# Optimization experiments

Hardware: AMD Instinct MI355X
Metric: run time of the kernel (lower is better)

## Reference

```python
import jax, jax.numpy as jnp
import numpy as np


def _morpho(x, weight, bias, sign, padding, stride):
    # x: [B,C,H,W], weight: [B,C,kh,kw], bias: [B,C], sign: [B]
    B, C, H, W = x.shape
    kh, kw = weight.shape[-2:]
    # sign handling: if |sign| >= 1e-7 multiply by sign, else leave unchanged
    m = (jnp.abs(sign) >= 1e-7).astype(x.dtype)          # [B], constant (detached in torch)
    s = m * sign + (1.0 - m)                              # effective multiplier per sample
    xs = x * s[:, None, None, None]
    # unfold zero-pads, and sign*0 == 0, so padding signed x with zeros is equivalent
    xp = jnp.pad(xs, ((0, 0), (0, 0), (padding, padding), (padding, padding)))
    H2 = (H + 2 * padding - kh) // stride + 1
    W2 = (W + 2 * padding - kw) // stride + 1
    # direct windowed max-plus: y[b,c,i,j] = max_{p,q} xs_pad[b,c,i*s+p,j*s+q] + w[b,c,p,q]
    # small fixed kh*kw loop avoids materializing the B*C*kh*kw*L unfold tensor
    y = jnp.full((B, C, H2, W2), -jnp.inf, dtype=x.dtype)
    for p in range(kh):
        for q in range(kw):
            patch = jax.lax.slice(
                xp,
                (0, 0, p, q),
                (B, C, p + (H2 - 1) * stride + 1, q + (W2 - 1) * stride + 1),
                (1, 1, stride, stride),
            )  # [B,C,H2,W2]
            y = jnp.maximum(y, patch + weight[:, :, p, q][:, :, None, None])
    y = y + bias[:, :, None, None]
    return y * s[:, None, None, None]


def setup_inputs() -> dict:
    key = jax.random.key(0)
    k1, k2, k3, k4 = jax.random.split(key, 4)
    B, C, H, W, kh, kw = 16, 64, 128, 128, 5, 5
    return {
        "x": jax.random.normal(k1, (B, C, H, W), dtype=jnp.float32),
        "weight": jax.random.normal(k2, (B, C, kh, kw), dtype=jnp.float32) * 0.1,
        "bias": jax.random.normal(k3, (B, C), dtype=jnp.float32) * 0.1,
        "sign": jax.random.normal(k4, (B,), dtype=jnp.float32),
        "padding": 2,
        "stride": 1,
    }


def reference(x, weight, bias, sign, padding, stride):
    return _morpho(x, weight, bias, sign, padding, stride)
```

## Files before the change

### kernel.cpp

```cpp
#include <hip/hip_runtime.h>
#include <math.h>
#include <stdint.h>

#define HH 128
#define WW 128
#define NFLOATS (16 * 64 * HH * WW)

typedef __fp16 h2 __attribute__((ext_vector_type(2)));

__device__ __forceinline__ h2 h2max(h2 a, h2 b) { return __builtin_elementwise_max(a, b); }
__device__ __forceinline__ uint32_t h2u(h2 v) { return __builtin_bit_cast(uint32_t, v); }
__device__ __forceinline__ h2 uh2(uint32_t v) { return __builtin_bit_cast(h2, v); }

#if __has_builtin(__builtin_elementwise_fma)
#define H2FMA(a, b, c) __builtin_elementwise_fma((a), (b), (c))
#else
#define H2FMA(a, b, c) ((a) * (b) + (c))
#endif

#define WAITV(n) do { asm volatile("s_waitcnt vmcnt(" #n ")" ::: "memory"); \
                      __builtin_amdgcn_sched_barrier(0); } while (0)

__global__ __launch_bounds__(256) void morpho_kernel(
    const float* __restrict__ x,
    const float* __restrict__ wgt,
    const float* __restrict__ bias,
    const float* __restrict__ sign,
    float* __restrict__ out)
{
    const int bid  = blockIdx.x;
    const int blk  = (bid & 7) * 512 + (bid >> 3);
    const int quad = blk & 3;
    const int bc   = blk >> 2;
    const int b    = bc >> 6;

    float*       __restrict__ yp = out + (size_t)bc * (HH * WW);
    const float* __restrict__ wp = wgt + bc * 25;

    const float sgn = sign[b];
    const float s   = (fabsf(sgn) >= 1e-7f) ? sgn : 1.0f;
    const float bvs = bias[bc] * s;
    const __fp16 sh = (__fp16)s;
    const h2 s2 = { sh, sh };

    uint32_t wsu[25];
#pragma unroll
    for (int k = 0; k < 25; ++k) {
        const __fp16 wh = (__fp16)wp[k];
        h2 w2 = { wh, wh };
        wsu[k] = (uint32_t)__builtin_amdgcn_readfirstlane((int)h2u(w2));
    }

    const int t  = threadIdx.x;
    const int tx = t & 31;
    const int ty = t >> 5;
    const int j0 = tx * 4;
    const int i0 = quad * 32 + ty * 4;
    const int planeOff = bc * (HH * WW);
    const bool mL = (tx > 0);
    const bool mR = (tx < 31);

    float2 vl[8]; float4 vm[8]; float2 vr[8];
    h2 acc0[4], acc1[4];

    auto ISSUE = [&](int r8) {
        const int rrow = i0 - 2 + r8;
        const int rc = min(max(rrow, 0), HH - 1);
        const int oM = planeOff + rc * WW + j0;
        const int oL = max(oM - 2, 0);
        const int oR = min(oM + 4, NFLOATS - 2);
        asm volatile("global_load_dwordx2 %0, %1, off" : "=v"(vl[r8]) : "v"(x + oL));
        asm volatile("global_load_dwordx4 %0, %1, off" : "=v"(vm[r8]) : "v"(x + oM));
        asm volatile("global_load_dwordx2 %0, %1, off" : "=v"(vr[r8]) : "v"(x + oR));
    };

    auto CONSUME = [&](int r8) {
        const int  rrow = i0 - 2 + r8;
        const bool rv = ((unsigned)rrow < (unsigned)HH);
        uint32_t e0 = h2u(__builtin_amdgcn_cvt_pkrtz(vl[r8].x, vl[r8].y));
        uint32_t e1 = h2u(__builtin_amdgcn_cvt_pkrtz(vm[r8].x, vm[r8].y));
        uint32_t e2 = h2u(__builtin_amdgcn_cvt_pkrtz(vm[r8].z, vm[r8].w));
        uint32_t e3 = h2u(__builtin_amdgcn_cvt_pkrtz(vr[r8].x, vr[r8].y));
        e0 = (rv && mL) ? e0 : 0u;
        e1 = rv ? e1 : 0u;
        e2 = rv ? e2 : 0u;
        e3 = (rv && mR) ? e3 : 0u;
        const uint32_t o0 = __builtin_amdgcn_alignbit(e1, e0, 16);
        const uint32_t o1 = __builtin_amdgcn_alignbit(e2, e1, 16);
        const uint32_t o2 = __builtin_amdgcn_alignbit(e3, e2, 16);
        const uint32_t P0[5] = { e0, o0, e1, o1, e2 };
        const uint32_t P1[5] = { e1, o1, e2, o2, e3 };
#pragma unroll
        for (int p = 0; p < 5; ++p) {
            const int oi = r8 - p;
            if (oi >= 0 && oi < 4) {
                const h2 w0 = uh2(wsu[p * 5 + 0]);
                const h2 w1 = uh2(wsu[p * 5 + 1]);
                const h2 w2 = uh2(wsu[p * 5 + 2]);
                const h2 w3 = uh2(wsu[p * 5 + 3]);
                const h2 w4 = uh2(wsu[p * 5 + 4]);
                {
                    const h2 t0 = H2FMA(uh2(P0[0]), s2, w0);
                    const h2 t1 = H2FMA(uh2(P0[1]), s2, w1);
                    const h2 t2 = H2FMA(uh2(P0[2]), s2, w2);
                    const h2 t3 = H2FMA(uh2(P0[3]), s2, w3);
                    const h2 t4 = H2FMA(uh2(P0[4]), s2, w4);
                    h2 mm = h2max(h2max(h2max(t0, t1), h2max(t2, t3)), t4);
                    acc0[oi] = (p == 0) ? mm : h2max(acc0[oi], mm);
                }
                {
                    const h2 t0 = H2FMA(uh2(P1[0]), s2, w0);
                    const h2 t1 = H2FMA(uh2(P1[1]), s2, w1);
                    const h2 t2 = H2FMA(uh2(P1[2]), s2, w2);
                    const h2 t3 = H2FMA(uh2(P1[3]), s2, w3);
                    const h2 t4 = H2FMA(uh2(P1[4]), s2, w4);
                    h2 mm = h2max(h2max(h2max(t0, t1), h2max(t2, t3)), t4);
                    acc1[oi] = (p == 0) ? mm : h2max(acc1[oi], mm);
                }
            }
        }
    };

    ISSUE(0); ISSUE(1); ISSUE(2); ISSUE(3);
    WAITV(9); CONSUME(0); ISSUE(4);
    WAITV(9); CONSUME(1); ISSUE(5);
    WAITV(9); CONSUME(2); ISSUE(6);
    WAITV(9); CONSUME(3); ISSUE(7);
    WAITV(9); CONSUME(4);
    WAITV(6); CONSUME(5);
    WAITV(3); CONSUME(6);
    WAITV(0); CONSUME(7);

#pragma unroll
    for (int a = 0; a < 4; ++a) {
        float4 o;
        o.x = fmaf((float)acc0[a][0], s, bvs);
        o.y = fmaf((float)acc0[a][1], s, bvs);
        o.z = fmaf((float)acc1[a][0], s, bvs);
        o.w = fmaf((float)acc1[a][1], s, bvs);
        *reinterpret_cast<float4*>(yp + (size_t)(i0 + a) * WW + j0) = o;
    }
}

extern "C" void kernel_launch(void* const* d_in, const int* in_sizes, int n_in,
                              void* d_out, int out_size, void* d_ws, size_t ws_size,
                              hipStream_t stream) {
    (void)d_ws; (void)ws_size; (void)in_sizes; (void)n_in; (void)out_size;
    const float* x    = (const float*)d_in[0];
    const float* w    = (const float*)d_in[1];
    const float* bias = (const float*)d_in[2];
    const float* sign = (const float*)d_in[3];
    float* out = (float*)d_out;

    morpho_kernel<<<4096, 256, 0, stream>>>(x, w, bias, sign, out);
}
```

Baseline: 29.92 us.

## Widen per-thread tile to 8 columns and fetch halo via lane shuffles

Each thread now computes a 4x8 output tile instead of 4x4, and the grid is halved to 2048 blocks. The left and right halo columns now come from neighbouring lanes through width-16 shuffles instead of extra overlapping dwordx2 loads, cutting redundant global load traffic and instructions. Input rows are held in a 4-deep register ring, and outputs are written with nontemporal stores to reduce cache pollution. In exchange there are more accumulators per thread, which may raise register pressure, and fewer waves to hide memory latency.

```diff
diff --git a/kernel.cpp b/kernel.cpp
--- a/kernel.cpp
+++ b/kernel.cpp
@@ -4,9 +4,9 @@
 
 #define HH 128
 #define WW 128
-#define NFLOATS (16 * 64 * HH * WW)
 
 typedef __fp16 h2 __attribute__((ext_vector_type(2)));
+typedef float  f4 __attribute__((ext_vector_type(4)));
 
 __device__ __forceinline__ h2 h2max(h2 a, h2 b) { return __builtin_elementwise_max(a, b); }
 __device__ __forceinline__ uint32_t h2u(h2 v) { return __builtin_bit_cast(uint32_t, v); }
@@ -29,9 +29,9 @@
     float* __restrict__ out)
 {
     const int bid  = blockIdx.x;
-    const int blk  = (bid & 7) * 512 + (bid >> 3);
-    const int quad = blk & 3;
-    const int bc   = blk >> 2;
+    const int blk  = (bid & 7) * 256 + (bid >> 3);
+    const int half = blk & 1;
+    const int bc   = blk >> 1;
     const int b    = bc >> 6;
 
     float*       __restrict__ yp = out + (size_t)bc * (HH * WW);
@@ -52,44 +52,47 @@
     }
 
     const int t  = threadIdx.x;
-    const int tx = t & 31;
-    const int ty = t >> 5;
-    const int j0 = tx * 4;
-    const int i0 = quad * 32 + ty * 4;
+    const int tx = t & 15;
+    const int ty = t >> 4;
+    const int j0 = tx * 8;
+    const int i0 = half * 64 + ty * 4;
     const int planeOff = bc * (HH * WW);
     const bool mL = (tx > 0);
-    const bool mR = (tx < 31);
+    const bool mR = (tx < 15);
 
-    float2 vl[8]; float4 vm[8]; float2 vr[8];
-    h2 acc0[4], acc1[4];
+    asm volatile("s_waitcnt vmcnt(0)" ::: "memory");
+
+    float4 va[4], vb[4];
+    h2 acc[4][4];
 
     auto ISSUE = [&](int r8) {
         const int rrow = i0 - 2 + r8;
-        const int rc = min(max(rrow, 0), HH - 1);
-        const int oM = planeOff + rc * WW + j0;
-        const int oL = max(oM - 2, 0);
-        const int oR = min(oM + 4, NFLOATS - 2);
-        asm volatile("global_load_dwordx2 %0, %1, off" : "=v"(vl[r8]) : "v"(x + oL));
-        asm volatile("global_load_dwordx4 %0, %1, off" : "=v"(vm[r8]) : "v"(x + oM));
-        asm volatile("global_load_dwordx2 %0, %1, off" : "=v"(vr[r8]) : "v"(x + oR));
+        const int rc   = min(max(rrow, 0), HH - 1);
+        const float* gp = x + planeOff + rc * WW + j0;
+        asm volatile("global_load_dwordx4 %0, %1, off" : "=v"(va[r8 & 3]) : "v"(gp));
+        asm volatile("global_load_dwordx4 %0, %1, off" : "=v"(vb[r8 & 3]) : "v"(gp + 4));
     };
 
     auto CONSUME = [&](int r8) {
         const int  rrow = i0 - 2 + r8;
         const bool rv = ((unsigned)rrow < (unsigned)HH);
-        uint32_t e0 = h2u(__builtin_amdgcn_cvt_pkrtz(vl[r8].x, vl[r8].y));
-        uint32_t e1 = h2u(__builtin_amdgcn_cvt_pkrtz(vm[r8].x, vm[r8].y));
-        uint32_t e2 = h2u(__builtin_amdgcn_cvt_pkrtz(vm[r8].z, vm[r8].w));
-        uint32_t e3 = h2u(__builtin_amdgcn_cvt_pkrtz(vr[r8].x, vr[r8].y));
-        e0 = (rv && mL) ? e0 : 0u;
-        e1 = rv ? e1 : 0u;
-        e2 = rv ? e2 : 0u;
-        e3 = (rv && mR) ? e3 : 0u;
-        const uint32_t o0 = __builtin_amdgcn_alignbit(e1, e0, 16);
-        const uint32_t o1 = __builtin_amdgcn_alignbit(e2, e1, 16);
-        const uint32_t o2 = __builtin_amdgcn_alignbit(e3, e2, 16);
-        const uint32_t P0[5] = { e0, o0, e1, o1, e2 };
-        const uint32_t P1[5] = { e1, o1, e2, o2, e3 };
+        const float4 u = va[r8 & 3];
+        const float4 v = vb[r8 & 3];
+        uint32_t E0 = h2u(__builtin_amdgcn_cvt_pkrtz(u.x, u.y));
+        uint32_t E1 = h2u(__builtin_amdgcn_cvt_pkrtz(u.z, u.w));
+        uint32_t E2 = h2u(__builtin_amdgcn_cvt_pkrtz(v.x, v.y));
+        uint32_t E3 = h2u(__builtin_amdgcn_cvt_pkrtz(v.z, v.w));
+        E0 = rv ? E0 : 0u;  E1 = rv ? E1 : 0u;
+        E2 = rv ? E2 : 0u;  E3 = rv ? E3 : 0u;
+        uint32_t eL = (uint32_t)__shfl_up((int)E3, 1, 16);
+        uint32_t eR = (uint32_t)__shfl_down((int)E0, 1, 16);
+        eL = mL ? eL : 0u;
+        eR = mR ? eR : 0u;
+        const uint32_t A[6] = { eL, E0, E1, E2, E3, eR };
+        uint32_t O[5];
+#pragma unroll
+        for (int k2 = 0; k2 < 5; ++k2) O[k2] = __builtin_amdgcn_alignbit(A[k2 + 1], A[k2], 16);
+
 #pragma unroll
         for (int p = 0; p < 5; ++p) {
             const int oi = r8 - p;
@@ -99,46 +102,44 @@
                 const h2 w2 = uh2(wsu[p * 5 + 2]);
                 const h2 w3 = uh2(wsu[p * 5 + 3]);
                 const h2 w4 = uh2(wsu[p * 5 + 4]);
-                {
-                    const h2 t0 = H2FMA(uh2(P0[0]), s2, w0);
-                    const h2 t1 = H2FMA(uh2(P0[1]), s2, w1);
-                    const h2 t2 = H2FMA(uh2(P0[2]), s2, w2);
-                    const h2 t3 = H2FMA(uh2(P0[3]), s2, w3);
-                    const h2 t4 = H2FMA(uh2(P0[4]), s2, w4);
+#pragma unroll
+                for (int i = 0; i < 4; ++i) {
+                    const h2 t0 = H2FMA(uh2(A[i]),     s2, w0);
+                    const h2 t1 = H2FMA(uh2(O[i]),     s2, w1);
+                    const h2 t2 = H2FMA(uh2(A[i + 1]), s2, w2);
+                    const h2 t3 = H2FMA(uh2(O[i + 1]), s2, w3);
+                    const h2 t4 = H2FMA(uh2(A[i + 2]), s2, w4);
                     h2 mm = h2max(h2max(h2max(t0, t1), h2max(t2, t3)), t4);
-                    acc0[oi] = (p == 0) ? mm : h2max(acc0[oi], mm);
-                }
-                {
-                    const h2 t0 = H2FMA(uh2(P1[0]), s2, w0);
-                    const h2 t1 = H2FMA(uh2(P1[1]), s2, w1);
-                    const h2 t2 = H2FMA(uh2(P1[2]), s2, w2);
-                    const h2 t3 = H2FMA(uh2(P1[3]), s2, w3);
-                    const h2 t4 = H2FMA(uh2(P1[4]), s2, w4);
-                    h2 mm = h2max(h2max(h2max(t0, t1), h2max(t2, t3)), t4);
-                    acc1[oi] = (p == 0) ? mm : h2max(acc1[oi], mm);
+                    acc[oi][i] = (p == 0) ? mm : h2max(acc[oi][i], mm);
                 }
             }
         }
     };
 
     ISSUE(0); ISSUE(1); ISSUE(2); ISSUE(3);
-    WAITV(9); CONSUME(0); ISSUE(4);
-    WAITV(9); CONSUME(1); ISSUE(5);
-    WAITV(9); CONSUME(2); ISSUE(6);
-    WAITV(9); CONSUME(3); ISSUE(7);
-    WAITV(9); CONSUME(4);
-    WAITV(6); CONSUME(5);
-    WAITV(3); CONSUME(6);
+    WAITV(6); CONSUME(0); ISSUE(4);
+    WAITV(6); CONSUME(1); ISSUE(5);
+    WAITV(6); CONSUME(2); ISSUE(6);
+    WAITV(6); CONSUME(3); ISSUE(7);
+    WAITV(6); CONSUME(4);
+    WAITV(4); CONSUME(5);
+    WAITV(2); CONSUME(6);
     WAITV(0); CONSUME(7);
 
 #pragma unroll
     for (int a = 0; a < 4; ++a) {
-        float4 o;
-        o.x = fmaf((float)acc0[a][0], s, bvs);
-        o.y = fmaf((float)acc0[a][1], s, bvs);
-        o.z = fmaf((float)acc1[a][0], s, bvs);
-        o.w = fmaf((float)acc1[a][1], s, bvs);
-        *reinterpret_cast<float4*>(yp + (size_t)(i0 + a) * WW + j0) = o;
+        float* rp = yp + (size_t)(i0 + a) * WW + j0;
+        f4 o01, o23;
+        o01.x = fmaf((float)acc[a][0][0], s, bvs);
+        o01.y = fmaf((float)acc[a][0][1], s, bvs);
+        o01.z = fmaf((float)acc[a][1][0], s, bvs);
+        o01.w = fmaf((float)acc[a][1][1], s, bvs);
+        o23.x = fmaf((float)acc[a][2][0], s, bvs);
+        o23.y = fmaf((float)acc[a][2][1], s, bvs);
+        o23.z = fmaf((float)acc[a][3][0], s, bvs);
+        o23.w = fmaf((float)acc[a][3][1], s, bvs);
+        __builtin_nontemporal_store(o01, reinterpret_cast<f4*>(rp));
+        __builtin_nontemporal_store(o23, reinterpret_cast<f4*>(rp + 4));
     }
 }
 
@@ -152,5 +153,5 @@
     const float* sign = (const float*)d_in[3];
     float* out = (float*)d_out;
 
-    morpho_kernel<<<4096, 256, 0, stream>>>(x, w, bias, sign, out);
+    morpho_kernel<<<2048, 256, 0, stream>>>(x, w, bias, sign, out);
 }
```

Result: slower. 32.67 us (+9.2%).
